# Kernel optimization log

Measured on AMD Instinct MI355X. Metric: run time of the kernel, lower is better.

## Reference

```python
import jax, jax.numpy as jnp
import numpy as np

B, OUT, IN = 2048, 4096, 4096
KEEPRATE = 0.5  # mid-training drop schedule state; first-call default masks nothing


def setup_inputs() -> dict:
    key = jax.random.key(0)
    k1, k2, k3, k4 = jax.random.split(key, 4)
    data = jax.random.normal(k1, (B, IN), dtype=jnp.float32)
    # weight parameter = fftn of a real N(0, 0.1) matrix, stored as complex
    w0 = jax.random.normal(k2, (OUT, IN), dtype=jnp.float32) * 0.1
    wc = jnp.fft.fftn(w0.astype(jnp.float32))
    w_real = jnp.real(wc).astype(jnp.float32)
    w_imag = jnp.imag(wc).astype(jnp.float32)
    bias = jax.random.normal(k3, (OUT,), dtype=jnp.float32) * 0.1
    # ZMAT: rank assignment, a permutation of 0..OUT*IN-1
    zmat = jax.random.permutation(k4, jnp.arange(OUT * IN, dtype=jnp.int64)).reshape(OUT, IN)
    return {"data": data, "w_real": w_real, "w_imag": w_imag, "bias": bias, "zmat": zmat}


def reference(data, w_real, w_imag, bias, zmat):
    O, I = w_real.shape
    numel = O * I
    threval = KEEPRATE * numel
    # IDROP: keep entries whose rank <= threshold (ZMAT > threval -> 0)
    idrop = (zmat.astype(jnp.float32) <= threval).astype(w_real.dtype)
    dropweight = (w_real + 1j * w_imag) * idrop  # masked FFT-domain weight
    # torch.fft.irfftn(dropweight, s=(O, I)): full ifft on dim 0, real irfft on dim 1
    # (numpy/jax irfft crops the last axis to I//2+1, same as torch)
    w_spatial = jnp.fft.irfftn(dropweight, s=(O, I), axes=(0, 1)).astype(data.dtype)
    return data @ w_spatial.T + bias
```

## Files before the change

### kernel.cpp

```cpp
#include <hip/hip_runtime.h>
#include <hip/hip_bf16.h>
#include <stdint.h>

#define OUT_N 4096
#define IN_N  4096
#define BATCH 2048
#define KHALF 2049

typedef __bf16 bf16x8 __attribute__((ext_vector_type(8)));
typedef float  f32x4  __attribute__((ext_vector_type(4)));

__device__ __forceinline__ unsigned short f2bf(float f) {
  unsigned int u = __builtin_bit_cast(unsigned int, f);
  u += 0x7FFFu + ((u >> 16) & 1u);
  return (unsigned short)(u >> 16);
}

__device__ __forceinline__ float2 cmul(float2 a, float2 b) {
  return make_float2(a.x * b.x - a.y * b.y, a.x * b.y + a.y * b.x);
}
__device__ __forceinline__ float2 cadd(float2 a, float2 b) { return make_float2(a.x + b.x, a.y + b.y); }
__device__ __forceinline__ float2 csub(float2 a, float2 b) { return make_float2(a.x - b.x, a.y - b.y); }
__device__ __forceinline__ float2 muli(float2 a) { return make_float2(-a.y, a.x); }

__device__ __forceinline__ void dft4i(float2& x0, float2& x1, float2& x2, float2& x3) {
  float2 t0 = cadd(x0, x2), t1 = csub(x0, x2);
  float2 t2 = cadd(x1, x3), t3 = csub(x1, x3);
  float2 it3 = muli(t3);
  x0 = cadd(t0, t2); x2 = csub(t0, t2);
  x1 = cadd(t1, it3); x3 = csub(t1, it3);
}

#define C8f  0.70710678118654752f
#define C16f 0.92387953251128676f
#define S16f 0.38268343236508977f

__device__ __forceinline__ void dft16i(float2 r[16]) {
  float2 t[16];
#pragma unroll
  for (int b = 0; b < 4; ++b) {
    float2 a0 = r[b], a1 = r[4 + b], a2 = r[8 + b], a3 = r[12 + b];
    dft4i(a0, a1, a2, a3);
    t[b * 4 + 0] = a0; t[b * 4 + 1] = a1; t[b * 4 + 2] = a2; t[b * 4 + 3] = a3;
  }
  const float2 W1 = make_float2(C16f, S16f);
  const float2 W2 = make_float2(C8f, C8f);
  const float2 W3 = make_float2(S16f, C16f);
  const float2 W6 = make_float2(-C8f, C8f);
  const float2 W9 = make_float2(-C16f, -S16f);
  t[5]  = cmul(t[5],  W1);  t[6]  = cmul(t[6],  W2);  t[7]  = cmul(t[7],  W3);
  t[9]  = cmul(t[9],  W2);  t[10] = muli(t[10]);      t[11] = cmul(t[11], W6);
  t[13] = cmul(t[13], W3);  t[14] = cmul(t[14], W6);  t[15] = cmul(t[15], W9);
#pragma unroll
  for (int q = 0; q < 4; ++q) {
    float2 a0 = t[q], a1 = t[4 + q], a2 = t[8 + q], a3 = t[12 + q];
    dft4i(a0, a1, a2, a3);
    r[q] = a0; r[q + 4] = a1; r[q + 8] = a2; r[q + 12] = a3;
  }
}

__device__ __forceinline__ void twiddle16(float2 r[16], float theta) {
  float sn, cs;
  __sincosf(theta, &sn, &cs);
  float2 w = make_float2(cs, sn);
  float2 wk = w;
  r[1] = cmul(r[1], wk);
#pragma unroll
  for (int k = 2; k < 16; ++k) {
    wk = cmul(wk, w);
    r[k] = cmul(r[k], wk);
  }
}

__device__ void fft4096_core(float2 r[16], float2* lds, int t) {
  dft16i(r);
  twiddle16(r, 1.53398078788564123e-3f * (float)t);
#pragma unroll
  for (int k1 = 0; k1 < 16; ++k1) lds[k1 * 256 + (t ^ k1)] = r[k1];
  __syncthreads();
  const int k1 = t & 15, b = t >> 4;
  float2 s[16];
#pragma unroll
  for (int a = 0; a < 16; ++a) s[a] = lds[k1 * 256 + ((16 * a + b) ^ k1)];
  __syncthreads();
  dft16i(s);
  twiddle16(s, 2.45436926061702596e-2f * (float)b);
#pragma unroll
  for (int c = 0; c < 16; ++c) lds[k1 * 256 + ((c * 16 + b) ^ k1)] = s[c];
  __syncthreads();
#pragma unroll
  for (int bb = 0; bb < 16; ++bb) r[bb] = lds[k1 * 256 + ((b * 16 + bb) ^ k1)];
  dft16i(r);
}

__global__ void mask_transpose(const float* __restrict__ wr, const float* __restrict__ wi,
                               const int* __restrict__ zmat, float2* __restrict__ wt) {
  __shared__ float2 tile[32][65];
  const int tx = threadIdx.x;
  const int ty = threadIdx.y;
  const int o0 = blockIdx.y * 32;
  if (blockIdx.x == 32) {
    int t = ty * 32 + tx;
    if (t < 32) {
      int o = o0 + t;
      size_t idx = (size_t)o * IN_N + 2048;
      float2 v = make_float2(0.f, 0.f);
      if (zmat[idx] <= 8388608) v = make_float2(wr[idx], wi[idx]);
      wt[(size_t)2048 * OUT_N + o] = v;
    }
    return;
  }
  const int k0 = blockIdx.x * 64;
#pragma unroll
  for (int r = 0; r < 4; ++r) {
    int o = o0 + ty + r * 8;
    size_t base = (size_t)o * IN_N + k0 + tx * 2;
    float2 vr = *(const float2*)&wr[base];
    float2 vi = *(const float2*)&wi[base];
    int2   z  = *(const int2*)&zmat[base];
    tile[ty + r * 8][tx * 2]     = (z.x <= 8388608) ? make_float2(vr.x, vi.x) : make_float2(0.f, 0.f);
    tile[ty + r * 8][tx * 2 + 1] = (z.y <= 8388608) ? make_float2(vr.y, vi.y) : make_float2(0.f, 0.f);
  }
  __syncthreads();
#pragma unroll
  for (int rr = 0; rr < 8; ++rr) {
    int k = k0 + ty + rr * 8;
    int o = o0 + tx;
    wt[(size_t)k * OUT_N + o] = tile[tx][ty + rr * 8];
  }
}

__global__ __launch_bounds__(256) void col_ifft(float2* __restrict__ wt) {
  __shared__ float2 lds[4096];
  const int t = threadIdx.x;
  float2* row = wt + (size_t)blockIdx.x * OUT_N;
  float2 r[16];
#pragma unroll
  for (int n1 = 0; n1 < 16; ++n1) r[n1] = row[n1 * 256 + t];
  fft4096_core(r, lds, t);
#pragma unroll
  for (int d = 0; d < 16; ++d) row[t + 256 * d] = r[d];
}

__global__ __launch_bounds__(256) void row_irfft2(const float2* __restrict__ wt,
                                                  unsigned short* __restrict__ wbf) {
  __shared__ float4 lsf[2048];
  const int t = threadIdx.x;
  const int bid = (int)blockIdx.x;
  const int lb  = (bid & 7) * 256 + (bid >> 3);
  const int oa = lb * 2, ob = oa + 1;
  const float4* wt4 = (const float4*)wt;
  const int oq = oa >> 1;
#pragma unroll
  for (int j = 0; j < 8; ++j) {
    int k = t + j * 256;
    lsf[k] = wt4[(size_t)k * 2048 + oq];
  }
  __syncthreads();
  float2 r[16];
#pragma unroll
  for (int n1 = 0; n1 < 16; ++n1) {
    int m = n1 * 256 + t;
    float2 za, zb;
    if (m == 0)        { float4 v = lsf[0];    za = make_float2(v.x, 0.f); zb = make_float2(v.z, 0.f); }
    else if (m < 2048) { float4 v = lsf[m];    za = make_float2(v.x, v.y); zb = make_float2(v.z, v.w); }
    else if (m == 2048){ float4 v = wt4[(size_t)2048 * 2048 + oq];
                         za = make_float2(v.x, 0.f); zb = make_float2(v.z, 0.f); }
    else { float4 v = lsf[4096 - m];
           za = make_float2(v.x, -v.y); zb = make_float2(v.z, -v.w); }
    r[n1] = make_float2(za.x - zb.y, za.y + zb.x);
  }
  __syncthreads();
  fft4096_core(r, (float2*)lsf, t);
  const float sc = 1.0f / (4096.0f * 4096.0f);
  unsigned short* orow_a = wbf + (size_t)oa * IN_N;
  unsigned short* orow_b = wbf + (size_t)ob * IN_N;
#pragma unroll
  for (int d = 0; d < 16; ++d) {
    orow_a[t + 256 * d] = f2bf(r[d].x * sc);
    orow_b[t + 256 * d] = f2bf(r[d].y * sc);
  }
}

__global__ void cvt_bf16(const float* __restrict__ x, unsigned short* __restrict__ o, int n4) {
  int i = blockIdx.x * blockDim.x + threadIdx.x;
  if (i < n4) {
    float4 v = ((const float4*)x)[i];
    ushort4 r;
    r.x = f2bf(v.x); r.y = f2bf(v.y); r.z = f2bf(v.z); r.w = f2bf(v.w);
    ((ushort4*)o)[i] = r;
  }
}

#define BK 64
#define NT (IN_N / BK)

__device__ __forceinline__ void gload_lds16(const void* gp, void* lp) {
  typedef const __attribute__((address_space(1))) void* gptr_t;
  typedef __attribute__((address_space(3))) void* lptr_t;
  __builtin_amdgcn_global_load_lds((gptr_t)(unsigned long long)gp,
                                   (lptr_t)(unsigned int)(unsigned long long)lp,
                                   16, 0, 0);
}

__device__ __forceinline__ void stage_tile(const unsigned short* __restrict__ A,
                                           const unsigned short* __restrict__ B,
                                           unsigned short* as, unsigned short* bs,
                                           int gm0, int gn0, int kt,
                                           int r0, int srow, int schunk) {
#pragma unroll
  for (int j = 0; j < 4; ++j) {
    gload_lds16(A + ((size_t)(gm0 + r0 + j * 8 + srow) * IN_N + kt + schunk * 8),
                as + (size_t)(r0 + j * 8) * BK);
    gload_lds16(B + ((size_t)(gn0 + r0 + j * 8 + srow) * IN_N + kt + schunk * 8),
                bs + (size_t)(r0 + j * 8) * BK);
  }
}

__global__ __launch_bounds__(256) void gemm_bt_bias(const unsigned short* __restrict__ A,
                                                    const unsigned short* __restrict__ B,
                                                    const float* __restrict__ bias,
                                                    float* __restrict__ C) {
  __shared__ __align__(16) unsigned short As[2][128 * BK];
  __shared__ __align__(16) unsigned short Bs[2][128 * BK];
  const int tid  = threadIdx.x;
  const int wave = tid >> 6;
  const int lane = tid & 63;
  const int gm0 = blockIdx.y * 128;
  const int gn0 = blockIdx.x * 128;

  f32x4 acc[4][4] = {};
  const int wm = wave >> 1, wn = wave & 1;
  const int srow   = lane >> 3;
  const int schunk = (lane & 7) ^ srow;
  const int r0     = wave * 32;
  const int l7 = lane & 7;
  const int qbase = lane >> 4;
  const int fra = wm * 64 + (lane & 15);
  const int frb = wn * 64 + (lane & 15);

  stage_tile(A, B, As[0], Bs[0], gm0, gn0, 0,  r0, srow, schunk);
  stage_tile(A, B, As[1], Bs[1], gm0, gn0, BK, r0, srow, schunk);

  for (int t = 0; t < NT; ++t) {
    const int S = t & 1;
    if (t < NT - 1) asm volatile("s_waitcnt vmcnt(8)" ::: "memory");
    else            asm volatile("s_waitcnt vmcnt(0)" ::: "memory");
    __builtin_amdgcn_sched_barrier(0);
    __builtin_amdgcn_s_barrier();
    __builtin_amdgcn_sched_barrier(0);

#pragma unroll
    for (int kk = 0; kk < 2; ++kk) {
      bf16x8 af[4], bfr[4];
      const int q = kk * 4 + qbase;
#pragma unroll
      for (int i = 0; i < 4; ++i) {
        af[i]  = *(const bf16x8*)&As[S][(fra + i * 16) * BK + ((q ^ l7) * 8)];
        bfr[i] = *(const bf16x8*)&Bs[S][(frb + i * 16) * BK + ((q ^ l7) * 8)];
      }
#pragma unroll
      for (int mi = 0; mi < 4; ++mi)
#pragma unroll
        for (int ni = 0; ni < 4; ++ni)
          acc[mi][ni] = __builtin_amdgcn_mfma_f32_16x16x32_bf16(af[mi], bfr[ni], acc[mi][ni], 0, 0, 0);
    }
    __builtin_amdgcn_sched_barrier(0);
    __builtin_amdgcn_s_barrier();
    if (t + 2 < NT)
      stage_tile(A, B, As[S], Bs[S], gm0, gn0, (t + 2) * BK, r0, srow, schunk);
  }

  const int col0 = gn0 + wn * 64 + (lane & 15);
  const int row0 = gm0 + wm * 64 + (lane >> 4) * 4;
#pragma unroll
  for (int mi = 0; mi < 4; ++mi) {
#pragma unroll
    for (int ni = 0; ni < 4; ++ni) {
      int col = col0 + ni * 16;
      float bv = bias[col];
#pragma unroll
      for (int r = 0; r < 4; ++r) {
        int row = row0 + mi * 16 + r;
        C[(size_t)row * OUT_N + col] = acc[mi][ni][r] + bv;
      }
    }
  }
}

extern "C" void kernel_launch(void* const* d_in, const int* in_sizes, int n_in,
                              void* d_out, int out_size, void* d_ws, size_t ws_size,
                              hipStream_t stream) {
  const float* data = (const float*)d_in[0];
  const float* wr   = (const float*)d_in[1];
  const float* wi   = (const float*)d_in[2];
  const float* bias = (const float*)d_in[3];
  const int*   zmat = (const int*)d_in[4];

  char* ws = (char*)d_ws;
  float2* wt = (float2*)ws;
  unsigned short* wbf = (unsigned short*)(ws + 67141632ull);
  unsigned short* dbf = (unsigned short*)(ws + 100696064ull);

  hipLaunchKernelGGL(mask_transpose, dim3(33, 128), dim3(32, 8), 0, stream, wr, wi, zmat, wt);
  hipLaunchKernelGGL(col_ifft,       dim3(2049),    dim3(256),   0, stream, wt);
  hipLaunchKernelGGL(row_irfft2,     dim3(2048),    dim3(256),   0, stream, wt, wbf);
  hipLaunchKernelGGL(cvt_bf16,       dim3(8192),    dim3(256),   0, stream, data, dbf, (BATCH * IN_N) / 4);
  hipLaunchKernelGGL(gemm_bt_bias,   dim3(OUT_N / 128, BATCH / 128), dim3(256), 0, stream,
                     dbf, wbf, bias, (float*)d_out);
}
```

Baseline: 328.7 us.

## Write column-IFFT output transposed so row IRFFT reads contiguous rows

The column IFFT now writes its results out of place into a pair-interleaved transposed buffer, with the Nyquist row sent to a scratch area inside the output. The row IRFFT can then load each output-row pair as one contiguous float4 row instead of doing a strided gather across k. The cost of non-contiguous access moves from the reads in row_irfft2 to the writes in col_ifft_t, which now scatter with a stride. Workspace buffers are reused to keep the extra buffer within the available space.

After: 350.0 us. 1.06x slower.

```diff
diff --git a/kernel.cpp b/kernel.cpp
--- a/kernel.cpp
+++ b/kernel.cpp
@@ -130,31 +130,45 @@
   }
 }
 
-__global__ __launch_bounds__(256) void col_ifft(float2* __restrict__ wt) {
+__global__ __launch_bounds__(256) void col_ifft_t(const float2* __restrict__ wt,
+                                                  float2* __restrict__ wtp2,
+                                                  float2* __restrict__ nyq2) {
   __shared__ float2 lds[4096];
   const int t = threadIdx.x;
-  float2* row = wt + (size_t)blockIdx.x * OUT_N;
+  const int bid = (int)blockIdx.x;
+  const bool ny = (bid == 2048);
+  const int kk = ny ? 2048 : ((bid & 7) * 256 + (bid >> 3));
+  const float2* row = wt + (size_t)kk * OUT_N;
   float2 r[16];
 #pragma unroll
   for (int n1 = 0; n1 < 16; ++n1) r[n1] = row[n1 * 256 + t];
   fft4096_core(r, lds, t);
-#pragma unroll
-  for (int d = 0; d < 16; ++d) row[t + 256 * d] = r[d];
-}
-
-__global__ __launch_bounds__(256) void row_irfft2(const float2* __restrict__ wt,
+  if (!ny) {
+    const size_t base = (size_t)kk * 2 + (t & 1);
+    const int Lt = t >> 1;
+#pragma unroll
+    for (int d = 0; d < 16; ++d) {
+      size_t L = (size_t)(Lt + 128 * d);
+      wtp2[L * 4096 + base] = r[d];
+    }
+  } else {
+#pragma unroll
+    for (int d = 0; d < 16; ++d) nyq2[t + 256 * d] = r[d];
+  }
+}
+
+__global__ __launch_bounds__(256) void row_irfft2(const float4* __restrict__ wtp,
+                                                  const float4* __restrict__ nyq,
                                                   unsigned short* __restrict__ wbf) {
   __shared__ float4 lsf[2048];
   const int t = threadIdx.x;
-  const int bid = (int)blockIdx.x;
-  const int lb  = (bid & 7) * 256 + (bid >> 3);
-  const int oa = lb * 2, ob = oa + 1;
-  const float4* wt4 = (const float4*)wt;
-  const int oq = oa >> 1;
+  const int L = (int)blockIdx.x;
+  const int oa = L * 2, ob = oa + 1;
+  const float4* src = wtp + (size_t)L * 2048;
 #pragma unroll
   for (int j = 0; j < 8; ++j) {
     int k = t + j * 256;
-    lsf[k] = wt4[(size_t)k * 2048 + oq];
+    lsf[k] = src[k];
   }
   __syncthreads();
   float2 r[16];
@@ -164,7 +178,7 @@
     float2 za, zb;
     if (m == 0)        { float4 v = lsf[0];    za = make_float2(v.x, 0.f); zb = make_float2(v.z, 0.f); }
     else if (m < 2048) { float4 v = lsf[m];    za = make_float2(v.x, v.y); zb = make_float2(v.z, v.w); }
-    else if (m == 2048){ float4 v = wt4[(size_t)2048 * 2048 + oq];
+    else if (m == 2048){ float4 v = nyq[L];
                          za = make_float2(v.x, 0.f); zb = make_float2(v.z, 0.f); }
     else { float4 v = lsf[4096 - m];
            za = make_float2(v.x, -v.y); zb = make_float2(v.z, -v.w); }
@@ -298,13 +312,15 @@
   const int*   zmat = (const int*)d_in[4];
 
   char* ws = (char*)d_ws;
-  float2* wt = (float2*)ws;
-  unsigned short* wbf = (unsigned short*)(ws + 67141632ull);
-  unsigned short* dbf = (unsigned short*)(ws + 100696064ull);
+  float2* wt  = (float2*)ws;
+  float4* wtp = (float4*)(ws + 67141632ull);
+  unsigned short* wbf = (unsigned short*)ws;
+  unsigned short* dbf = (unsigned short*)(ws + 33554432ull);
+  float2* nyq2 = (float2*)d_out;
 
   hipLaunchKernelGGL(mask_transpose, dim3(33, 128), dim3(32, 8), 0, stream, wr, wi, zmat, wt);
-  hipLaunchKernelGGL(col_ifft,       dim3(2049),    dim3(256),   0, stream, wt);
-  hipLaunchKernelGGL(row_irfft2,     dim3(2048),    dim3(256),   0, stream, wt, wbf);
+  hipLaunchKernelGGL(col_ifft_t,     dim3(2049),    dim3(256),   0, stream, wt, (float2*)wtp, nyq2);
+  hipLaunchKernelGGL(row_irfft2,     dim3(2048),    dim3(256),   0, stream, wtp, (const float4*)d_out, wbf);
   hipLaunchKernelGGL(cvt_bf16,       dim3(8192),    dim3(256),   0, stream, data, dbf, (BATCH * IN_N) / 4);
   hipLaunchKernelGGL(gemm_bt_bias,   dim3(OUT_N / 128, BATCH / 128), dim3(256), 0, stream,
                      dbf, wbf, bias, (float*)d_out);
```
